# Kernel tuning notes

Hardware: AMD Instinct MI355X
Metric: run time of the kernel (lower is better)

Reference implementation:

```python
import jax, jax.numpy as jnp
import numpy as np

BS, RAL, LAL = 128, 1024, 256
CS, VOC, HFS, EMB = 256, 34, 512, 256


def setup_inputs() -> dict:
    key0 = jax.random.key(0)
    ks = jax.random.split(key0, 16)
    s = 0.02
    # mask from random valid lengths (at least 1 valid frame per example)
    lengths = jax.random.randint(ks[15], (BS,), RAL // 2, RAL + 1)
    mask = (jnp.arange(RAL)[None, :] < lengths[:, None]).astype(jnp.float32)
    return {
        "key": jax.random.normal(ks[0], (BS, RAL, CS), jnp.float32),
        "val": jax.random.normal(ks[1], (BS, RAL, CS), jnp.float32),
        "mask": mask,
        "emb": jax.random.normal(ks[2], (VOC, EMB), jnp.float32) * s,
        "Wih_a": jax.random.normal(ks[3], (4 * HFS, EMB + CS), jnp.float32) * s,
        "Whh_a": jax.random.normal(ks[4], (4 * HFS, HFS), jnp.float32) * s,
        "bih_a": jnp.zeros((4 * HFS,), jnp.float32),
        "bhh_a": jnp.zeros((4 * HFS,), jnp.float32),
        "Wih_b": jax.random.normal(ks[5], (4 * HFS, HFS), jnp.float32) * s,
        "Whh_b": jax.random.normal(ks[6], (4 * HFS, HFS), jnp.float32) * s,
        "bih_b": jnp.zeros((4 * HFS,), jnp.float32),
        "bhh_b": jnp.zeros((4 * HFS,), jnp.float32),
        "Wq": jax.random.normal(ks[7], (CS, HFS), jnp.float32) * s,
        "bq": jnp.zeros((CS,), jnp.float32),
        "Wc": jax.random.normal(ks[8], (VOC, HFS + CS), jnp.float32) * s,
        "bc": jnp.zeros((VOC,), jnp.float32),
        "y": jax.random.randint(ks[9], (BS, LAL), 0, VOC, jnp.int32),
    }


def _lstm_cell(x, h, c, Wih, Whh, bih, bhh):
    z = x @ Wih.T + bih + h @ Whh.T + bhh  # (BS, 4H)
    i, f, g, o = jnp.split(z, 4, axis=-1)
    i, f, o = jax.nn.sigmoid(i), jax.nn.sigmoid(f), jax.nn.sigmoid(o)
    g = jnp.tanh(g)
    c2 = f * c + i * g
    return o * jnp.tanh(c2), c2


def _attend(key, val, query, mask):
    # energy: (BS, RAL) = bmm(key, query[...,None])
    energy = jnp.einsum("brc,bc->br", key, query)
    att = jax.nn.softmax(energy, axis=1) * mask
    att = att / jnp.sum(att, axis=1, keepdims=True)
    return jnp.einsum("br,brc->bc", att, val)  # context (BS, CS)


def reference(key, val, mask, emb, Wih_a, Whh_a, bih_a, bhh_a,
              Wih_b, Whh_b, bih_b, bhh_b, Wq, bq, Wc, bc, y):
    bs = y.shape[0]
    z = jnp.zeros((bs, HFS), jnp.float32)
    init = (z, z, z, z, jnp.zeros((bs, CS), jnp.float32))

    def step(carry, y_t):
        ha, ca, hb, cb, ctx = carry
        e = emb[y_t]  # (BS, EMB)
        x = jnp.concatenate([e, ctx], axis=1)
        ha, ca = _lstm_cell(x, ha, ca, Wih_a, Whh_a, bih_a, bhh_a)
        hb, cb = _lstm_cell(ha, hb, cb, Wih_b, Whh_b, bih_b, bhh_b)
        query = hb @ Wq.T + bq  # (BS, CS)
        ctx = _attend(key, val, query, mask)
        logits = jnp.concatenate([hb, ctx], axis=1) @ Wc.T + bc  # (BS, VOC)
        return (ha, ca, hb, cb, ctx), logits

    _, preds = jax.lax.scan(step, init, y.T)  # (LAL, BS, VOC)
    return jnp.transpose(preds, (1, 0, 2))  # (BS, LAL, VOC)
```

## Files before the change

### kernel.cpp

```cpp
#include <hip/hip_runtime.h>
#include <cstdint>
#include <cstddef>

static constexpr int BS  = 128;
static constexpr int RAL = 1024;
static constexpr int LAL = 256;
static constexpr int CS  = 256;
static constexpr int VOC = 34;
static constexpr int HFS = 512;
static constexpr int EMB = 256;

static constexpr int NSPLIT = 2;
static constexpr int RSPL   = RAL / NSPLIT;
static constexpr int NBLK   = 256;

typedef float  f32x4  __attribute__((ext_vector_type(4)));
typedef short  bf16x8 __attribute__((ext_vector_type(8)));

#define SC_AGENT __HIP_MEMORY_SCOPE_AGENT

static __device__ __forceinline__ float bflo(unsigned int u) {
    return __builtin_bit_cast(float, u << 16);
}
static __device__ __forceinline__ float bfhi(unsigned int u) {
    return __builtin_bit_cast(float, u & 0xffff0000u);
}
static __device__ __forceinline__ unsigned short f2bf(float f) {
    unsigned int x = __builtin_bit_cast(unsigned int, f);
    x = (x + 0x7fffu + ((x >> 16) & 1u)) >> 16;
    return (unsigned short)x;
}
static __device__ __forceinline__ float bcf(unsigned u) { return __builtin_bit_cast(float, u); }
static __device__ __forceinline__ unsigned fcb(float f) { return __builtin_bit_cast(unsigned, f); }
static __device__ __forceinline__ float sigf(float x)   { return 1.0f / (1.0f + __expf(-x)); }
static __device__ __forceinline__ float tanhf_(float x) { return 1.0f - 2.0f / (__expf(2.0f * x) + 1.0f); }

static __device__ __forceinline__ unsigned ldu32(const void* p) {
    return __hip_atomic_load((const unsigned*)p, __ATOMIC_RELAXED, SC_AGENT);
}
static __device__ __forceinline__ unsigned long long ldu64(const void* p) {
    return __hip_atomic_load((const unsigned long long*)p, __ATOMIC_RELAXED, SC_AGENT);
}
static __device__ __forceinline__ void stu32(void* p, unsigned v) {
    __hip_atomic_store((unsigned*)p, v, __ATOMIC_RELAXED, SC_AGENT);
}
static __device__ __forceinline__ void stu64(void* p, unsigned long long v) {
    __hip_atomic_store((unsigned long long*)p, v, __ATOMIC_RELAXED, SC_AGENT);
}
static __device__ __forceinline__ bf16x8 ld_bf16x8_sys(const unsigned short* p) {
    union { unsigned long long q[2]; bf16x8 v; } u;
    u.q[0] = ldu64(p);
    u.q[1] = ldu64(p + 4);
    return u.v;
}
static __device__ __forceinline__ unsigned long long packbf4(float a, float b, float c, float d) {
    return (unsigned long long)f2bf(a)
         | ((unsigned long long)f2bf(b) << 16)
         | ((unsigned long long)f2bf(c) << 32)
         | ((unsigned long long)f2bf(d) << 48);
}

__global__ void cvt4_kernel(const float4* __restrict__ in, ushort4* __restrict__ out, int n4) {
    int i  = blockIdx.x * blockDim.x + threadIdx.x;
    int st = gridDim.x * blockDim.x;
    for (; i < n4; i += st) {
        float4 v = in[i];
        ushort4 o;
        o.x = f2bf(v.x); o.y = f2bf(v.y); o.z = f2bf(v.z); o.w = f2bf(v.w);
        out[i] = o;
    }
}

__global__ __launch_bounds__(256) void len_kernel(const float* __restrict__ mask,
                                                  int* __restrict__ Llen,
                                                  float* __restrict__ attS) {
    __shared__ int red[256];
    const int b = blockIdx.x, tid = threadIdx.x;
    int c = 0;
    for (int r = tid; r < RAL; r += 256) c += (mask[b * RAL + r] != 0.0f) ? 1 : 0;
    red[tid] = c;
    __syncthreads();
    for (int s = 128; s > 0; s >>= 1) {
        if (tid < s) red[tid] += red[tid + s];
        __syncthreads();
    }
    if (tid == 0) Llen[b] = red[0];
    if (tid < NSPLIT) attS[b * NSPLIT + tid] = 0.5f;
}

struct SmLstm {
    float zp[7][4][64][4];
    float hT[16][17];
};
struct SmAttn {
    float hb_l[HFS];
    float q_lds[CS];
    float e_lds[RSPL];
    float ctxp[8][CS];
    float red[16];
};
static constexpr size_t SMSZ = sizeof(SmLstm) > sizeof(SmAttn) ? sizeof(SmLstm) : sizeof(SmAttn);

struct PParams {
    const void* keyp; const void* valp;
    const int* Llen; const int* y;
    const unsigned short* embb;
    const unsigned short* WihA; const unsigned short* WhhA;
    const float* bihA; const float* bhhA;
    const unsigned short* WihB; const unsigned short* WhhB;
    const float* bihB; const float* bhhB;
    const unsigned short* Wqb; const float* bq;
    const float* Wc; const float* bc;
    unsigned short* ha; unsigned short* hbuf;
    float* ca; float* cbuf;
    float* attM; float* attS; float* attC;
    unsigned* grp; unsigned* root;
    float* outp;
};

static __device__ __forceinline__ void gbar(unsigned* grp, unsigned* root, int blk, int round) {
    asm volatile("s_waitcnt vmcnt(0) lgkmcnt(0)" ::: "memory");
    __syncthreads();
    if (threadIdx.x == 0) {
        unsigned* g = grp + (blk >> 4) * 32;
        unsigned old = __hip_atomic_fetch_add(g, 1u, __ATOMIC_RELAXED, SC_AGENT);
        if (old == (unsigned)(round * 16 + 15))
            __hip_atomic_fetch_add(root, 1u, __ATOMIC_RELAXED, SC_AGENT);
        const unsigned tgt = (unsigned)((round + 1) * 16);
        while (__hip_atomic_load(root, __ATOMIC_RELAXED, SC_AGENT) < tgt)
            __builtin_amdgcn_s_sleep(8);
    }
    __syncthreads();
}

static __device__ __forceinline__ bf16x8 ctx_merge8(const float* c0, const float* c1,
                                                    float w0, float w1) {
    union { unsigned short s[8]; bf16x8 v; } r;
#pragma unroll
    for (int g = 0; g < 4; ++g) {
        unsigned long long qa = ldu64(c0 + g * 2);
        unsigned long long qb = ldu64(c1 + g * 2);
        float ax = bcf((unsigned)qa), ay = bcf((unsigned)(qa >> 32));
        float bx = bcf((unsigned)qb), by = bcf((unsigned)(qb >> 32));
        r.s[g * 2 + 0] = f2bf(w0 * ax + w1 * bx);
        r.s[g * 2 + 1] = f2bf(w0 * ay + w1 * by);
    }
    return r.v;
}

template <bool ISA>
static __device__ __forceinline__ void lstm_phase(
    int blk, int tid,
    const unsigned short* xrow,
    const float* attM, const float* attS, const float* attC,
    const unsigned short* embb, const int* yidx, int t,
    const unsigned short* hIn,
    const unsigned short* Wih, const unsigned short* Whh,
    const float* bih, const float* bhh,
    float* cst, unsigned short* hout,
    SmLstm* sm)
{
    const int lane = tid & 63;
    const int wv   = tid >> 6;
    const int seg  = wv >> 1;
    const int sub  = wv & 1;
    const int quad = lane >> 4;
    const int l16  = lane & 15;
    const int jsl  = blk & 31;
    const int bgr  = blk >> 5;
    const int j    = jsl * 16 + l16;
    const int mrow = bgr * 16 + l16;
    const int off0 = sub * 128 + quad * 8;

    const unsigned short* arow = nullptr;
    const float* c0 = nullptr;
    float w0m = 0.0f, w1m = 0.0f;
    bool scA;
    if (seg >= 2) {
        arow = hIn + (long)mrow * HFS + (seg & 1) * 256 + off0;
        scA = true;
    } else if (!ISA) {
        arow = xrow + (long)mrow * HFS + (seg & 1) * 256 + off0;
        scA = true;
    } else if (seg == 0) {
        arow = embb + (long)yidx[mrow * LAL + t] * EMB + off0;
        scA = false;
    } else {
        c0 = attC + (long)mrow * NSPLIT * CS + off0;
        float M0 = bcf(ldu32(attM + mrow * 2)),     M1 = bcf(ldu32(attM + mrow * 2 + 1));
        float S0 = bcf(ldu32(attS + mrow * 2)),     S1 = bcf(ldu32(attS + mrow * 2 + 1));
        float mm = fmaxf(M0, M1);
        float e0 = __expf(M0 - mm), e1 = __expf(M1 - mm);
        float inv = 1.0f / (e0 * S0 + e1 * S1);
        w0m = e0 * inv; w1m = e1 * inv;
        scA = false;
    }

    const unsigned short* wb = ((seg < 2) ? Wih : Whh) + (seg & 1) * 256 + off0;
    const unsigned short* wg[4];
#pragma unroll
    for (int g = 0; g < 4; ++g) wg[g] = wb + (long)(g * HFS + j) * HFS;

    f32x4 acc[4];
#pragma unroll
    for (int g = 0; g < 4; ++g) acc[g] = (f32x4)0.0f;

#pragma unroll
    for (int kc = 0; kc < 4; ++kc) {
        bf16x8 a;
        if (scA)                 a = ld_bf16x8_sys(arow + kc * 32);
        else if (!ISA || seg == 0) a = *(const bf16x8*)(arow + kc * 32);
        else                     a = ctx_merge8(c0 + kc * 32, c0 + CS + kc * 32, w0m, w1m);
        bf16x8 b0 = *(const bf16x8*)(wg[0] + kc * 32);
        bf16x8 b1 = *(const bf16x8*)(wg[1] + kc * 32);
        bf16x8 b2 = *(const bf16x8*)(wg[2] + kc * 32);
        bf16x8 b3 = *(const bf16x8*)(wg[3] + kc * 32);
        acc[0] = __builtin_amdgcn_mfma_f32_16x16x32_bf16(a, b0, acc[0], 0, 0, 0);
        acc[1] = __builtin_amdgcn_mfma_f32_16x16x32_bf16(a, b1, acc[1], 0, 0, 0);
        acc[2] = __builtin_amdgcn_mfma_f32_16x16x32_bf16(a, b2, acc[2], 0, 0, 0);
        acc[3] = __builtin_amdgcn_mfma_f32_16x16x32_bf16(a, b3, acc[3], 0, 0, 0);
    }

    if (wv != 0) {
#pragma unroll
        for (int g = 0; g < 4; ++g)
            *(f32x4*)&sm->zp[wv - 1][g][lane][0] = acc[g];
    }
    __syncthreads();
    if (wv == 0) {
#pragma unroll
        for (int g = 0; g < 4; ++g) {
#pragma unroll
            for (int w = 0; w < 7; ++w)
                acc[g] += *(const f32x4*)&sm->zp[w][g][lane][0];
        }
        const float bI = bih[j]           + bhh[j];
        const float bF = bih[HFS + j]     + bhh[HFS + j];
        const float bG = bih[2 * HFS + j] + bhh[2 * HFS + j];
        const float bO = bih[3 * HFS + j] + bhh[3 * HFS + j];
#pragma unroll
        for (int r = 0; r < 4; ++r) {
            int m   = bgr * 16 + quad * 4 + r;
            int idx = m * HFS + j;
            float iv = sigf(acc[0][r] + bI);
            float fv = sigf(acc[1][r] + bF);
            float gv = tanhf_(acc[2][r] + bG);
            float ov = sigf(acc[3][r] + bO);
            float cn = fv * cst[idx] + iv * gv;
            cst[idx] = cn;
            sm->hT[quad * 4 + r][l16] = ov * tanhf_(cn);
        }
        float h0 = sm->hT[l16][quad * 4 + 0];
        float h1 = sm->hT[l16][quad * 4 + 1];
        float h2 = sm->hT[l16][quad * 4 + 2];
        float h3 = sm->hT[l16][quad * 4 + 3];
        stu64(hout + (long)(bgr * 16 + l16) * HFS + jsl * 16 + quad * 4,
              packbf4(h0, h1, h2, h3));
    }
}

template <bool KVBF>
static __device__ __forceinline__ void attn_phase(
    int blk, int tid,
    const void* keyp, const void* valp,
    const int* __restrict__ Llen,
    const unsigned short* __restrict__ hbv,
    const unsigned short* __restrict__ Wqb, const float* __restrict__ bq,
    float* __restrict__ attM, float* __restrict__ attS, float* __restrict__ attC,
    SmAttn* sm)
{
    const int b     = blk >> 1;
    const int sp    = blk & 1;
    const int L     = Llen[b];
    const int rhalf = (L + 1) >> 1;
    const int rbase = sp * rhalf;
    int nv = L - rbase;
    if (nv > rhalf) nv = rhalf;

    if (nv <= 0) {
        if (tid < CS) stu32(attC + ((long)b * NSPLIT + sp) * CS + tid, fcb(0.0f));
        if (tid == 0) {
            stu32(attM + b * NSPLIT + sp, fcb(-1e30f));
            stu32(attS + b * NSPLIT + sp, fcb(0.0f));
        }
        return;
    }

    if (tid < 128) {
        unsigned long long q = ldu64(hbv + (long)b * HFS + tid * 4);
        sm->hb_l[tid * 4 + 0] = bflo((unsigned)(q       ) & 0xffffu ? (unsigned)(q) & 0xffffu : 0u);
        sm->hb_l[tid * 4 + 0] = bflo((unsigned)(q        & 0xffffu));
        sm->hb_l[tid * 4 + 1] = bflo((unsigned)((q >> 16) & 0xffffu));
        sm->hb_l[tid * 4 + 2] = bflo((unsigned)((q >> 32) & 0xffffu));
        sm->hb_l[tid * 4 + 3] = bflo((unsigned)((q >> 48) & 0xffffu));
    }
    __syncthreads();

    {
        const int c  = tid >> 1;
        const int jj = tid & 1;
        const unsigned short* wr = Wqb + (long)c * HFS + jj * 256;
        const float* xr = &sm->hb_l[jj * 256];
        float qa = 0.0f;
#pragma unroll 8
        for (int k = 0; k < 256; k += 8) {
            uint4 u = *(const uint4*)(wr + k);
            float4 h0 = *(const float4*)(xr + k);
            float4 h1 = *(const float4*)(xr + k + 4);
            qa += bflo(u.x) * h0.x + bfhi(u.x) * h0.y
                + bflo(u.y) * h0.z + bfhi(u.y) * h0.w
                + bflo(u.z) * h1.x + bfhi(u.z) * h1.y
                + bflo(u.w) * h1.z + bfhi(u.w) * h1.w;
        }
        qa += __shfl_xor(qa, 1);
        if (jj == 0) sm->q_lds[c] = qa + bq[c];
    }
    __syncthreads();

    {
        const int jj   = tid & 7;
        const int rloc = tid >> 3;
        for (int r0 = 0; r0 < nv; r0 += 64) {
            const int r = r0 + rloc;
            float acc = 0.0f;
            if (r < nv) {
                if (KVBF) {
                    const unsigned short* kp = (const unsigned short*)keyp
                        + ((long)b * RAL + rbase + r) * CS + jj * 32;
#pragma unroll
                    for (int i = 0; i < 4; ++i) {
                        uint4 u = *(const uint4*)(kp + i * 8);
                        const float* qp = &sm->q_lds[jj * 32 + i * 8];
                        float4 qa  = *(const float4*)qp;
                        float4 qb2 = *(const float4*)(qp + 4);
                        acc += bflo(u.x) * qa.x  + bfhi(u.x) * qa.y
                             + bflo(u.y) * qa.z  + bfhi(u.y) * qa.w
                             + bflo(u.z) * qb2.x + bfhi(u.z) * qb2.y
                             + bflo(u.w) * qb2.z + bfhi(u.w) * qb2.w;
                    }
                } else {
                    const float* kp = (const float*)keyp
                        + ((long)b * RAL + rbase + r) * CS + jj * 32;
#pragma unroll
                    for (int i = 0; i < 8; ++i) {
                        float4 kv = *(const float4*)(kp + i * 4);
                        float4 qa = *(const float4*)&sm->q_lds[jj * 32 + i * 4];
                        acc += kv.x * qa.x + kv.y * qa.y + kv.z * qa.z + kv.w * qa.w;
                    }
                }
            }
            acc += __shfl_xor(acc, 1);
            acc += __shfl_xor(acc, 2);
            acc += __shfl_xor(acc, 4);
            if (jj == 0 && r < nv) sm->e_lds[r] = acc;
        }
    }
    __syncthreads();

    float pm = (tid < nv) ? sm->e_lds[tid] : -1e30f;
#pragma unroll
    for (int s = 32; s > 0; s >>= 1) pm = fmaxf(pm, __shfl_xor(pm, s));
    if ((tid & 63) == 0) sm->red[tid >> 6] = pm;
    __syncthreads();
    float M = sm->red[0];
#pragma unroll
    for (int i = 1; i < 8; ++i) M = fmaxf(M, sm->red[i]);

    float ps = 0.0f;
    if (tid < nv) { float v = __expf(sm->e_lds[tid] - M); sm->e_lds[tid] = v; ps = v; }
#pragma unroll
    for (int s = 32; s > 0; s >>= 1) ps += __shfl_xor(ps, s);
    if ((tid & 63) == 0) sm->red[8 + (tid >> 6)] = ps;
    __syncthreads();
    float S = 0.0f;
#pragma unroll
    for (int i = 0; i < 8; ++i) S += sm->red[8 + i];

    if (tid == 0) {
        stu32(attM + b * NSPLIT + sp, fcb(M));
        stu32(attS + b * NSPLIT + sp, fcb(S));
    }

    {
        const int wv = tid >> 6;
        const int c4 = (tid & 63) * 4;
        float a0 = 0.f, a1 = 0.f, a2 = 0.f, a3 = 0.f;
        if (KVBF) {
            const unsigned short* vb = (const unsigned short*)valp
                + ((long)b * RAL + rbase) * CS + c4;
            int r = wv;
            for (; r + 24 < nv; r += 32) {
                uint2 u0 = *(const uint2*)(vb + (long)(r)      * CS);
                uint2 u1 = *(const uint2*)(vb + (long)(r + 8)  * CS);
                uint2 u2 = *(const uint2*)(vb + (long)(r + 16) * CS);
                uint2 u3 = *(const uint2*)(vb + (long)(r + 24) * CS);
                float w0 = sm->e_lds[r],      w1 = sm->e_lds[r + 8];
                float w2 = sm->e_lds[r + 16], w3 = sm->e_lds[r + 24];
                a0 += w0 * bflo(u0.x) + w1 * bflo(u1.x) + w2 * bflo(u2.x) + w3 * bflo(u3.x);
                a1 += w0 * bfhi(u0.x) + w1 * bfhi(u1.x) + w2 * bfhi(u2.x) + w3 * bfhi(u3.x);
                a2 += w0 * bflo(u0.y) + w1 * bflo(u1.y) + w2 * bflo(u2.y) + w3 * bflo(u3.y);
                a3 += w0 * bfhi(u0.y) + w1 * bfhi(u1.y) + w2 * bfhi(u2.y) + w3 * bfhi(u3.y);
            }
            for (; r < nv; r += 8) {
                uint2 u = *(const uint2*)(vb + (long)r * CS);
                float w = sm->e_lds[r];
                a0 += w * bflo(u.x); a1 += w * bfhi(u.x);
                a2 += w * bflo(u.y); a3 += w * bfhi(u.y);
            }
        } else {
            const float* vb = (const float*)valp + ((long)b * RAL + rbase) * CS + c4;
            int r = wv;
            for (; r + 24 < nv; r += 32) {
                float4 v0 = *(const float4*)(vb + (long)(r)      * CS);
                float4 v1 = *(const float4*)(vb + (long)(r + 8)  * CS);
                float4 v2 = *(const float4*)(vb + (long)(r + 16) * CS);
                float4 v3 = *(const float4*)(vb + (long)(r + 24) * CS);
                float w0 = sm->e_lds[r],      w1 = sm->e_lds[r + 8];
                float w2 = sm->e_lds[r + 16], w3 = sm->e_lds[r + 24];
                a0 += w0 * v0.x + w1 * v1.x + w2 * v2.x + w3 * v3.x;
                a1 += w0 * v0.y + w1 * v1.y + w2 * v2.y + w3 * v3.y;
                a2 += w0 * v0.z + w1 * v1.z + w2 * v2.z + w3 * v3.z;
                a3 += w0 * v0.w + w1 * v1.w + w2 * v2.w + w3 * v3.w;
            }
            for (; r < nv; r += 8) {
                float4 v = *(const float4*)(vb + (long)r * CS);
                float w = sm->e_lds[r];
                a0 += w * v.x; a1 += w * v.y; a2 += w * v.z; a3 += w * v.w;
            }
        }
        float4 out4 = {a0, a1, a2, a3};
        *(float4*)&sm->ctxp[tid >> 6][c4] = out4;
    }
    __syncthreads();

    if (tid < CS) {
        float cv = 0.0f;
#pragma unroll
        for (int w = 0; w < 8; ++w) cv += sm->ctxp[w][tid];
        stu32(attC + ((long)b * NSPLIT + sp) * CS + tid, fcb(cv));
    }
}

static __device__ __forceinline__ void logits_phase(
    int blk, int tid,
    const unsigned short* __restrict__ hb,
    const float* __restrict__ attM, const float* __restrict__ attS,
    const float* __restrict__ attC,
    const float* __restrict__ Wc, const float* __restrict__ bc,
    float* __restrict__ outp, int tOut)
{
    const int bgr  = blk >> 5;
    const int vsl  = blk & 31;
    const int bloc = tid >> 5;
    const int jj   = tid & 31;
    const int b    = bgr * 16 + bloc;

    float M0 = bcf(ldu32(attM + b * 2)),     M1 = bcf(ldu32(attM + b * 2 + 1));
    float S0 = bcf(ldu32(attS + b * 2)),     S1 = bcf(ldu32(attS + b * 2 + 1));
    float mm = fmaxf(M0, M1);
    float w0 = __expf(M0 - mm), w1 = __expf(M1 - mm);
    float inv = 1.0f / (w0 * S0 + w1 * S1);
    w0 *= inv; w1 *= inv;

    float xh[16];
    const unsigned short* hp = hb + (long)b * HFS + jj * 16;
#pragma unroll
    for (int g = 0; g < 4; ++g) {
        unsigned long long q = ldu64(hp + g * 4);
        xh[g * 4 + 0] = bflo((unsigned)( q        & 0xffffu));
        xh[g * 4 + 1] = bflo((unsigned)((q >> 16) & 0xffffu));
        xh[g * 4 + 2] = bflo((unsigned)((q >> 32) & 0xffffu));
        xh[g * 4 + 3] = bflo((unsigned)((q >> 48) & 0xffffu));
    }
    float xc[8];
    const float* c0 = attC + ((long)b * NSPLIT + 0) * CS + jj * 8;
    const float* c1 = attC + ((long)b * NSPLIT + 1) * CS + jj * 8;
#pragma unroll
    for (int g = 0; g < 4; ++g) {
        unsigned long long qa = ldu64(c0 + g * 2);
        unsigned long long qb = ldu64(c1 + g * 2);
        xc[g * 2 + 0] = w0 * bcf((unsigned)qa)         + w1 * bcf((unsigned)qb);
        xc[g * 2 + 1] = w0 * bcf((unsigned)(qa >> 32)) + w1 * bcf((unsigned)(qb >> 32));
    }

#pragma unroll
    for (int vv = 0; vv < 2; ++vv) {
        int v = vsl + vv * 32;
        if (v >= VOC) break;
        const float* wr = Wc + (long)v * (HFS + CS);
        float part = 0.0f;
#pragma unroll
        for (int g = 0; g < 4; ++g) {
            float4 wv4 = *(const float4*)(wr + jj * 16 + g * 4);
            part += wv4.x * xh[g * 4 + 0] + wv4.y * xh[g * 4 + 1]
                  + wv4.z * xh[g * 4 + 2] + wv4.w * xh[g * 4 + 3];
        }
#pragma unroll
        for (int g = 0; g < 2; ++g) {
            float4 wv4 = *(const float4*)(wr + HFS + jj * 8 + g * 4);
            part += wv4.x * xc[g * 4 + 0] + wv4.y * xc[g * 4 + 1]
                  + wv4.z * xc[g * 4 + 2] + wv4.w * xc[g * 4 + 3];
        }
        part += __shfl_xor(part, 1);
        part += __shfl_xor(part, 2);
        part += __shfl_xor(part, 4);
        part += __shfl_xor(part, 8);
        part += __shfl_xor(part, 16);
        if (jj == 0)
            outp[((long)b * LAL + tOut) * VOC + v] = part + bc[v];
    }
}

template <bool KVBF>
__global__ __launch_bounds__(512) void fused_kernel(PParams P)
{
    __shared__ __align__(16) unsigned char smraw[SMSZ];
    SmLstm* smL = (SmLstm*)smraw;
    SmAttn* smA = (SmAttn*)smraw;

    const int blk = blockIdx.x;
    const int tid = threadIdx.x;
    int round = 0;

    for (int t = 0; t < LAL; ++t) {
        const unsigned short* haIn  = P.ha   + (t & 1) * (BS * HFS);
        unsigned short*       haOut = P.ha   + ((t + 1) & 1) * (BS * HFS);
        const unsigned short* hbIn  = P.hbuf + (t & 1) * (BS * HFS);
        unsigned short*       hbOut = P.hbuf + ((t + 1) & 1) * (BS * HFS);

        lstm_phase<true>(blk, tid, nullptr, P.attM, P.attS, P.attC,
                         P.embb, P.y, t, haIn,
                         P.WihA, P.WhhA, P.bihA, P.bhhA, P.ca, haOut, smL);
        gbar(P.grp, P.root, blk, round++);

        if (t > 0)
            logits_phase(blk, tid, hbIn, P.attM, P.attS, P.attC, P.Wc, P.bc, P.outp, t - 1);
        lstm_phase<false>(blk, tid, haOut, nullptr, nullptr, nullptr,
                          nullptr, nullptr, t, hbIn,
                          P.WihB, P.WhhB, P.bihB, P.bhhB, P.cbuf, hbOut, smL);
        gbar(P.grp, P.root, blk, round++);

        attn_phase<KVBF>(blk, tid, P.keyp, P.valp, P.Llen, hbOut,
                         P.Wqb, P.bq, P.attM, P.attS, P.attC, smA);
        gbar(P.grp, P.root, blk, round++);
    }
    logits_phase(blk, tid, P.hbuf + (LAL & 1) * (BS * HFS),
                 P.attM, P.attS, P.attC, P.Wc, P.bc, P.outp, LAL - 1);
}

extern "C" void kernel_launch(void* const* d_in, const int* in_sizes, int n_in,
                              void* d_out, int out_size, void* d_ws, size_t ws_size,
                              hipStream_t stream)
{
    (void)in_sizes; (void)n_in; (void)out_size;
    const float* keyf  = (const float*)d_in[0];
    const float* valf  = (const float*)d_in[1];
    const float* mask  = (const float*)d_in[2];
    const float* embf  = (const float*)d_in[3];
    const float* WihAf = (const float*)d_in[4];
    const float* WhhAf = (const float*)d_in[5];
    const float* bihA  = (const float*)d_in[6];
    const float* bhhA  = (const float*)d_in[7];
    const float* WihBf = (const float*)d_in[8];
    const float* WhhBf = (const float*)d_in[9];
    const float* bihB  = (const float*)d_in[10];
    const float* bhhB  = (const float*)d_in[11];
    const float* Wqf   = (const float*)d_in[12];
    const float* bq    = (const float*)d_in[13];
    const float* Wc    = (const float*)d_in[14];
    const float* bc    = (const float*)d_in[15];
    const int*   y     = (const int*)d_in[16];
    float* outp = (float*)d_out;

    size_t off = 0;
    auto take = [&](size_t bytes) -> void* {
        void* p = (char*)d_ws + off;
        off += (bytes + 255) & ~(size_t)255;
        return p;
    };

    unsigned short* ha    = (unsigned short*)take((size_t)2 * BS * HFS * 2);
    unsigned short* hbuf  = (unsigned short*)take((size_t)2 * BS * HFS * 2);
    float*          ca    = (float*)take((size_t)BS * HFS * 4);
    float*          cbuf  = (float*)take((size_t)BS * HFS * 4);
    float*          attM  = (float*)take((size_t)BS * NSPLIT * 4);
    float*          attS  = (float*)take((size_t)BS * NSPLIT * 4);
    float*          attC  = (float*)take((size_t)BS * NSPLIT * CS * 4);
    unsigned*       grp   = (unsigned*)take((size_t)16 * 32 * 4);
    unsigned*       root  = (unsigned*)take((size_t)32 * 4);
    size_t stateBytes = off;

    int*            Llen  = (int*)take((size_t)BS * 4);
    unsigned short* embb  = (unsigned short*)take((size_t)VOC * EMB * 2);
    unsigned short* WihAb = (unsigned short*)take((size_t)4 * HFS * HFS * 2);
    unsigned short* WhhAb = (unsigned short*)take((size_t)4 * HFS * HFS * 2);
    unsigned short* WihBb = (unsigned short*)take((size_t)4 * HFS * HFS * 2);
    unsigned short* WhhBb = (unsigned short*)take((size_t)4 * HFS * HFS * 2);
    unsigned short* Wqb   = (unsigned short*)take((size_t)CS * HFS * 2);

    const size_t kvBytes = (size_t)BS * RAL * CS * 2;
    unsigned short* keyb = nullptr;
    unsigned short* valb = nullptr;
    bool kvbf = false;
    bool keyInVal = false;
    if (off + 2 * (kvBytes + 256) <= ws_size) {
        keyb = (unsigned short*)take(kvBytes);
        valb = (unsigned short*)take(kvBytes);
        kvbf = true;
    } else if (off + kvBytes + 256 <= ws_size) {
        valb = (unsigned short*)take(kvBytes);
        keyb = (unsigned short*)d_in[1];
        kvbf = true;
        keyInVal = true;
    }

    hipMemsetAsync(d_ws, 0, stateBytes, stream);
    len_kernel<<<dim3(BS), dim3(256), 0, stream>>>(mask, Llen, attS);

    auto cvt = [&](const float* src, unsigned short* dst, long n) {
        int n4 = (int)(n / 4);
        int blocks = (n4 + 255) / 256;
        if (blocks > 8192) blocks = 8192;
        cvt4_kernel<<<dim3(blocks), dim3(256), 0, stream>>>((const float4*)src, (ushort4*)dst, n4);
    };
    cvt(embf,  embb,  (long)VOC * EMB);
    cvt(WihAf, WihAb, (long)4 * HFS * HFS);
    cvt(WhhAf, WhhAb, (long)4 * HFS * HFS);
    cvt(WihBf, WihBb, (long)4 * HFS * HFS);
    cvt(WhhBf, WhhBb, (long)4 * HFS * HFS);
    cvt(Wqf,   Wqb,   (long)CS * HFS);
    if (kvbf) {
        if (keyInVal) {
            cvt(valf, valb, (long)BS * RAL * CS);
            cvt(keyf, keyb, (long)BS * RAL * CS);
        } else {
            cvt(keyf, keyb, (long)BS * RAL * CS);
            cvt(valf, valb, (long)BS * RAL * CS);
        }
    }

    PParams prm;
    prm.keyp = kvbf ? (const void*)keyb : (const void*)keyf;
    prm.valp = kvbf ? (const void*)valb : (const void*)valf;
    prm.Llen = Llen; prm.y = y;
    prm.embb = embb;
    prm.WihA = WihAb; prm.WhhA = WhhAb; prm.bihA = bihA; prm.bhhA = bhhA;
    prm.WihB = WihBb; prm.WhhB = WhhBb; prm.bihB = bihB; prm.bhhB = bhhB;
    prm.Wqb = Wqb; prm.bq = bq; prm.Wc = Wc; prm.bc = bc;
    prm.ha = ha; prm.hbuf = hbuf; prm.ca = ca; prm.cbuf = cbuf;
    prm.attM = attM; prm.attS = attS; prm.attC = attC;
    prm.grp = grp; prm.root = root;
    prm.outp = outp;

    void* kargs[] = { &prm };
    if (kvbf)
        hipLaunchCooperativeKernel(reinterpret_cast<void*>(&fused_kernel<true>),
                                   dim3(NBLK), dim3(512), kargs, 0, stream);
    else
        hipLaunchCooperativeKernel(reinterpret_cast<void*>(&fused_kernel<false>),
                                   dim3(NBLK), dim3(512), kargs, 0, stream);
}
```

Before: 13.00 ms.

## Double block size, add KV cache-warming waves and split query GEMM into MFMA phase

```diff
diff --git a/kernel.cpp b/kernel.cpp
--- a/kernel.cpp
+++ b/kernel.cpp
@@ -85,7 +85,7 @@
         __syncthreads();
     }
     if (tid == 0) Llen[b] = red[0];
-    if (tid < NSPLIT) attS[b * NSPLIT + tid] = 0.5f;
+    if (tid < NSPLIT) attS[b * NSPLIT + tid] = 1.0f / NSPLIT;
 }
 
 struct SmLstm {
@@ -93,11 +93,10 @@
     float hT[16][17];
 };
 struct SmAttn {
-    float hb_l[HFS];
     float q_lds[CS];
     float e_lds[RSPL];
-    float ctxp[8][CS];
-    float red[16];
+    float ctxp[32][CS];
+    float red[32];
 };
 static constexpr size_t SMSZ = sizeof(SmLstm) > sizeof(SmAttn) ? sizeof(SmLstm) : sizeof(SmAttn);
 
@@ -114,6 +113,7 @@
     unsigned short* ha; unsigned short* hbuf;
     float* ca; float* cbuf;
     float* attM; float* attS; float* attC;
+    float* qbuf;
     unsigned* grp; unsigned* root;
     float* outp;
 };
@@ -133,19 +133,43 @@
     __syncthreads();
 }
 
-static __device__ __forceinline__ bf16x8 ctx_merge8(const float* c0, const float* c1,
-                                                    float w0, float w1) {
+static __device__ __forceinline__ bf16x8 ctx_merge8(const float* cb, const float* wm) {
     union { unsigned short s[8]; bf16x8 v; } r;
 #pragma unroll
-    for (int g = 0; g < 4; ++g) {
-        unsigned long long qa = ldu64(c0 + g * 2);
-        unsigned long long qb = ldu64(c1 + g * 2);
-        float ax = bcf((unsigned)qa), ay = bcf((unsigned)(qa >> 32));
-        float bx = bcf((unsigned)qb), by = bcf((unsigned)(qb >> 32));
-        r.s[g * 2 + 0] = f2bf(w0 * ax + w1 * bx);
-        r.s[g * 2 + 1] = f2bf(w0 * ay + w1 * by);
+    for (int e = 0; e < 8; e += 2) {
+        float x0 = 0.f, x1 = 0.f;
+#pragma unroll
+        for (int s2 = 0; s2 < NSPLIT; ++s2) {
+            unsigned long long q = ldu64(cb + (long)s2 * CS + e);
+            x0 += wm[s2] * bcf((unsigned)q);
+            x1 += wm[s2] * bcf((unsigned)(q >> 32));
+        }
+        r.s[e]     = f2bf(x0);
+        r.s[e + 1] = f2bf(x1);
     }
     return r.v;
+}
+
+template <bool KVBF>
+static __device__ __forceinline__ void kv_touch(int blk, const void* ptr,
+                                                const int* __restrict__ Llen,
+                                                int rr, int rstride, int cc, int budget)
+{
+    if (!KVBF) return;
+    const int b = blk >> 1, sp = blk & 1;
+    const int L = Llen[b];
+    const int rhalf = (L + 1) >> 1;
+    const int rbase = sp * rhalf;
+    int nv = L - rbase; if (nv > rhalf) nv = rhalf;
+    if (nv > budget) nv = budget;
+    const uint4* kp = (const uint4*)((const unsigned short*)ptr
+                      + ((long)b * RAL + rbase) * CS) + cc;
+    unsigned acc = 0;
+    for (int r = rr; r < nv; r += rstride) {
+        uint4 u = kp[(long)r * 32];
+        acc ^= u.x ^ u.y ^ u.z ^ u.w;
+    }
+    asm volatile("" :: "v"(acc));
 }
 
 template <bool ISA>
@@ -162,69 +186,82 @@
 {
     const int lane = tid & 63;
     const int wv   = tid >> 6;
-    const int seg  = wv >> 1;
-    const int sub  = wv & 1;
+    const bool act = (wv < 8);
     const int quad = lane >> 4;
     const int l16  = lane & 15;
     const int jsl  = blk & 31;
     const int bgr  = blk >> 5;
     const int j    = jsl * 16 + l16;
     const int mrow = bgr * 16 + l16;
-    const int off0 = sub * 128 + quad * 8;
-
-    const unsigned short* arow = nullptr;
-    const float* c0 = nullptr;
-    float w0m = 0.0f, w1m = 0.0f;
-    bool scA;
-    if (seg >= 2) {
-        arow = hIn + (long)mrow * HFS + (seg & 1) * 256 + off0;
-        scA = true;
-    } else if (!ISA) {
-        arow = xrow + (long)mrow * HFS + (seg & 1) * 256 + off0;
-        scA = true;
-    } else if (seg == 0) {
-        arow = embb + (long)yidx[mrow * LAL + t] * EMB + off0;
-        scA = false;
-    } else {
-        c0 = attC + (long)mrow * NSPLIT * CS + off0;
-        float M0 = bcf(ldu32(attM + mrow * 2)),     M1 = bcf(ldu32(attM + mrow * 2 + 1));
-        float S0 = bcf(ldu32(attS + mrow * 2)),     S1 = bcf(ldu32(attS + mrow * 2 + 1));
-        float mm = fmaxf(M0, M1);
-        float e0 = __expf(M0 - mm), e1 = __expf(M1 - mm);
-        float inv = 1.0f / (e0 * S0 + e1 * S1);
-        w0m = e0 * inv; w1m = e1 * inv;
-        scA = false;
-    }
-
-    const unsigned short* wb = ((seg < 2) ? Wih : Whh) + (seg & 1) * 256 + off0;
-    const unsigned short* wg[4];
-#pragma unroll
-    for (int g = 0; g < 4; ++g) wg[g] = wb + (long)(g * HFS + j) * HFS;
 
     f32x4 acc[4];
 #pragma unroll
     for (int g = 0; g < 4; ++g) acc[g] = (f32x4)0.0f;
 
-#pragma unroll
-    for (int kc = 0; kc < 4; ++kc) {
-        bf16x8 a;
-        if (scA)                 a = ld_bf16x8_sys(arow + kc * 32);
-        else if (!ISA || seg == 0) a = *(const bf16x8*)(arow + kc * 32);
-        else                     a = ctx_merge8(c0 + kc * 32, c0 + CS + kc * 32, w0m, w1m);
-        bf16x8 b0 = *(const bf16x8*)(wg[0] + kc * 32);
-        bf16x8 b1 = *(const bf16x8*)(wg[1] + kc * 32);
-        bf16x8 b2 = *(const bf16x8*)(wg[2] + kc * 32);
-        bf16x8 b3 = *(const bf16x8*)(wg[3] + kc * 32);
-        acc[0] = __builtin_amdgcn_mfma_f32_16x16x32_bf16(a, b0, acc[0], 0, 0, 0);
-        acc[1] = __builtin_amdgcn_mfma_f32_16x16x32_bf16(a, b1, acc[1], 0, 0, 0);
-        acc[2] = __builtin_amdgcn_mfma_f32_16x16x32_bf16(a, b2, acc[2], 0, 0, 0);
-        acc[3] = __builtin_amdgcn_mfma_f32_16x16x32_bf16(a, b3, acc[3], 0, 0, 0);
-    }
-
-    if (wv != 0) {
-#pragma unroll
-        for (int g = 0; g < 4; ++g)
-            *(f32x4*)&sm->zp[wv - 1][g][lane][0] = acc[g];
+    if (act) {
+        const int seg  = wv >> 1;
+        const int sub  = wv & 1;
+        const int off0 = sub * 128 + quad * 8;
+
+        const unsigned short* arow = nullptr;
+        const float* c0 = nullptr;
+        float wm[NSPLIT];
+        bool scA;
+        if (seg >= 2) {
+            arow = hIn + (long)mrow * HFS + (seg & 1) * 256 + off0;
+            scA = true;
+        } else if (!ISA) {
+            arow = xrow + (long)mrow * HFS + (seg & 1) * 256 + off0;
+            scA = true;
+        } else if (seg == 0) {
+            arow = embb + (long)yidx[mrow * LAL + t] * EMB + off0;
+            scA = false;
+        } else {
+            c0 = attC + (long)mrow * NSPLIT * CS + off0;
+            float Ms[NSPLIT], Ss[NSPLIT];
+#pragma unroll
+            for (int s = 0; s < NSPLIT; ++s) {
+                Ms[s] = bcf(ldu32(attM + mrow * NSPLIT + s));
+                Ss[s] = bcf(ldu32(attS + mrow * NSPLIT + s));
+            }
+            float mm = Ms[0];
+#pragma unroll
+            for (int s = 1; s < NSPLIT; ++s) mm = fmaxf(mm, Ms[s]);
+            float den = 0.f;
+#pragma unroll
+            for (int s = 0; s < NSPLIT; ++s) { wm[s] = __expf(Ms[s] - mm); den += wm[s] * Ss[s]; }
+            float inv = 1.0f / den;
+#pragma unroll
+            for (int s = 0; s < NSPLIT; ++s) wm[s] *= inv;
+            scA = false;
+        }
+
+        const unsigned short* wb = ((seg < 2) ? Wih : Whh) + (seg & 1) * 256 + off0;
+        const unsigned short* wg[4];
+#pragma unroll
+        for (int g = 0; g < 4; ++g) wg[g] = wb + (long)(g * HFS + j) * HFS;
+
+#pragma unroll
+        for (int kc = 0; kc < 4; ++kc) {
+            bf16x8 a;
+            if (scA)                   a = ld_bf16x8_sys(arow + kc * 32);
+            else if (!ISA || seg == 0) a = *(const bf16x8*)(arow + kc * 32);
+            else                       a = ctx_merge8(c0 + kc * 32, wm);
+            bf16x8 b0 = *(const bf16x8*)(wg[0] + kc * 32);
+            bf16x8 b1 = *(const bf16x8*)(wg[1] + kc * 32);
+            bf16x8 b2 = *(const bf16x8*)(wg[2] + kc * 32);
+            bf16x8 b3 = *(const bf16x8*)(wg[3] + kc * 32);
+            acc[0] = __builtin_amdgcn_mfma_f32_16x16x32_bf16(a, b0, acc[0], 0, 0, 0);
+            acc[1] = __builtin_amdgcn_mfma_f32_16x16x32_bf16(a, b1, acc[1], 0, 0, 0);
+            acc[2] = __builtin_amdgcn_mfma_f32_16x16x32_bf16(a, b2, acc[2], 0, 0, 0);
+            acc[3] = __builtin_amdgcn_mfma_f32_16x16x32_bf16(a, b3, acc[3], 0, 0, 0);
+        }
+
+        if (wv != 0) {
+#pragma unroll
+            for (int g = 0; g < 4; ++g)
+                *(f32x4*)&sm->zp[wv - 1][g][lane][0] = acc[g];
+        }
     }
     __syncthreads();
     if (wv == 0) {
@@ -259,13 +296,55 @@
     }
 }
 
+static __device__ __forceinline__ void qcalc_phase(
+    int blk, int tid,
+    const unsigned short* hb,
+    const unsigned short* Wqb, const float* bq,
+    float* qbuf, SmLstm* sm)
+{
+    const int lane = tid & 63;
+    const int wv   = tid >> 6;
+    const bool act = (wv < 8);
+    const int quad = lane >> 4;
+    const int l16  = lane & 15;
+    const int mt   = blk >> 4;
+    const int nt   = blk & 15;
+
+    f32x4 acc = (f32x4)0.0f;
+    if (act) {
+        const int mrow = mt * 16 + l16;
+        const int c    = nt * 16 + l16;
+        const int koff = wv * 64 + quad * 8;
+        const unsigned short* ar = hb  + (long)mrow * HFS + koff;
+        const unsigned short* br = Wqb + (long)c    * HFS + koff;
+#pragma unroll
+        for (int kc = 0; kc < 2; ++kc) {
+            bf16x8 a = ld_bf16x8_sys(ar + kc * 32);
+            bf16x8 b = *(const bf16x8*)(br + kc * 32);
+            acc = __builtin_amdgcn_mfma_f32_16x16x32_bf16(a, b, acc, 0, 0, 0);
+        }
+        if (wv != 0) *(f32x4*)&sm->zp[wv - 1][0][lane][0] = acc;
+    }
+    __syncthreads();
+    if (wv == 0) {
+#pragma unroll
+        for (int w = 0; w < 7; ++w) acc += *(const f32x4*)&sm->zp[w][0][lane][0];
+        const int c = nt * 16 + l16;
+        const float bqv = bq[c];
+#pragma unroll
+        for (int r = 0; r < 4; ++r) {
+            int b2 = mt * 16 + quad * 4 + r;
+            stu32(qbuf + (long)b2 * CS + c, fcb(acc[r] + bqv));
+        }
+    }
+}
+
 template <bool KVBF>
 static __device__ __forceinline__ void attn_phase(
     int blk, int tid,
     const void* keyp, const void* valp,
     const int* __restrict__ Llen,
-    const unsigned short* __restrict__ hbv,
-    const unsigned short* __restrict__ Wqb, const float* __restrict__ bq,
+    const float* __restrict__ qbuf,
     float* __restrict__ attM, float* __restrict__ attS, float* __restrict__ attC,
     SmAttn* sm)
 {
@@ -286,51 +365,23 @@
         return;
     }
 
-    if (tid < 128) {
-        unsigned long long q = ldu64(hbv + (long)b * HFS + tid * 4);
-        sm->hb_l[tid * 4 + 0] = bflo((unsigned)(q       ) & 0xffffu ? (unsigned)(q) & 0xffffu : 0u);
-        sm->hb_l[tid * 4 + 0] = bflo((unsigned)(q        & 0xffffu));
-        sm->hb_l[tid * 4 + 1] = bflo((unsigned)((q >> 16) & 0xffffu));
-        sm->hb_l[tid * 4 + 2] = bflo((unsigned)((q >> 32) & 0xffffu));
-        sm->hb_l[tid * 4 + 3] = bflo((unsigned)((q >> 48) & 0xffffu));
-    }
+    if (tid < CS) sm->q_lds[tid] = bcf(ldu32(qbuf + (long)b * CS + tid));
     __syncthreads();
 
     {
-        const int c  = tid >> 1;
-        const int jj = tid & 1;
-        const unsigned short* wr = Wqb + (long)c * HFS + jj * 256;
-        const float* xr = &sm->hb_l[jj * 256];
-        float qa = 0.0f;
-#pragma unroll 8
-        for (int k = 0; k < 256; k += 8) {
-            uint4 u = *(const uint4*)(wr + k);
-            float4 h0 = *(const float4*)(xr + k);
-            float4 h1 = *(const float4*)(xr + k + 4);
-            qa += bflo(u.x) * h0.x + bfhi(u.x) * h0.y
-                + bflo(u.y) * h0.z + bfhi(u.y) * h0.w
-                + bflo(u.z) * h1.x + bfhi(u.z) * h1.y
-                + bflo(u.w) * h1.z + bfhi(u.w) * h1.w;
-        }
-        qa += __shfl_xor(qa, 1);
-        if (jj == 0) sm->q_lds[c] = qa + bq[c];
-    }
-    __syncthreads();
-
-    {
-        const int jj   = tid & 7;
-        const int rloc = tid >> 3;
-        for (int r0 = 0; r0 < nv; r0 += 64) {
+        const int jj   = tid & 3;
+        const int rloc = tid >> 2;
+        for (int r0 = 0; r0 < nv; r0 += 256) {
             const int r = r0 + rloc;
             float acc = 0.0f;
             if (r < nv) {
                 if (KVBF) {
                     const unsigned short* kp = (const unsigned short*)keyp
-                        + ((long)b * RAL + rbase + r) * CS + jj * 32;
-#pragma unroll
-                    for (int i = 0; i < 4; ++i) {
+                        + ((long)b * RAL + rbase + r) * CS + jj * 64;
+#pragma unroll
+                    for (int i = 0; i < 8; ++i) {
                         uint4 u = *(const uint4*)(kp + i * 8);
-                        const float* qp = &sm->q_lds[jj * 32 + i * 8];
+                        const float* qp = &sm->q_lds[jj * 64 + i * 8];
                         float4 qa  = *(const float4*)qp;
                         float4 qb2 = *(const float4*)(qp + 4);
                         acc += bflo(u.x) * qa.x  + bfhi(u.x) * qa.y
@@ -340,18 +391,17 @@
                     }
                 } else {
                     const float* kp = (const float*)keyp
-                        + ((long)b * RAL + rbase + r) * CS + jj * 32;
-#pragma unroll
-                    for (int i = 0; i < 8; ++i) {
+                        + ((long)b * RAL + rbase + r) * CS + jj * 64;
+#pragma unroll
+                    for (int i = 0; i < 16; ++i) {
                         float4 kv = *(const float4*)(kp + i * 4);
-                        float4 qa = *(const float4*)&sm->q_lds[jj * 32 + i * 4];
+                        float4 qa = *(const float4*)&sm->q_lds[jj * 64 + i * 4];
                         acc += kv.x * qa.x + kv.y * qa.y + kv.z * qa.z + kv.w * qa.w;
                     }
                 }
             }
             acc += __shfl_xor(acc, 1);
             acc += __shfl_xor(acc, 2);
-            acc += __shfl_xor(acc, 4);
             if (jj == 0 && r < nv) sm->e_lds[r] = acc;
         }
     }
@@ -364,17 +414,17 @@
     __syncthreads();
     float M = sm->red[0];
 #pragma unroll
-    for (int i = 1; i < 8; ++i) M = fmaxf(M, sm->red[i]);
+    for (int i = 1; i < 16; ++i) M = fmaxf(M, sm->red[i]);
 
     float ps = 0.0f;
     if (tid < nv) { float v = __expf(sm->e_lds[tid] - M); sm->e_lds[tid] = v; ps = v; }
 #pragma unroll
     for (int s = 32; s > 0; s >>= 1) ps += __shfl_xor(ps, s);
-    if ((tid & 63) == 0) sm->red[8 + (tid >> 6)] = ps;
+    if ((tid & 63) == 0) sm->red[16 + (tid >> 6)] = ps;
     __syncthreads();
     float S = 0.0f;
 #pragma unroll
-    for (int i = 0; i < 8; ++i) S += sm->red[8 + i];
+    for (int i = 0; i < 16; ++i) S += sm->red[16 + i];
 
     if (tid == 0) {
         stu32(attM + b * NSPLIT + sp, fcb(M));
@@ -382,61 +432,88 @@
     }
 
     {
-        const int wv = tid >> 6;
-        const int c4 = (tid & 63) * 4;
-        float a0 = 0.f, a1 = 0.f, a2 = 0.f, a3 = 0.f;
+        const int rg = tid >> 5;
+        const int c8 = (tid & 31) * 8;
+        float a0=0.f,a1=0.f,a2=0.f,a3=0.f,a4=0.f,a5=0.f,a6=0.f,a7=0.f;
         if (KVBF) {
             const unsigned short* vb = (const unsigned short*)valp
-                + ((long)b * RAL + rbase) * CS + c4;
-            int r = wv;
-            for (; r + 24 < nv; r += 32) {
-                uint2 u0 = *(const uint2*)(vb + (long)(r)      * CS);
-                uint2 u1 = *(const uint2*)(vb + (long)(r + 8)  * CS);
-                uint2 u2 = *(const uint2*)(vb + (long)(r + 16) * CS);
-                uint2 u3 = *(const uint2*)(vb + (long)(r + 24) * CS);
-                float w0 = sm->e_lds[r],      w1 = sm->e_lds[r + 8];
-                float w2 = sm->e_lds[r + 16], w3 = sm->e_lds[r + 24];
-                a0 += w0 * bflo(u0.x) + w1 * bflo(u1.x) + w2 * bflo(u2.x) + w3 * bflo(u3.x);
-                a1 += w0 * bfhi(u0.x) + w1 * bfhi(u1.x) + w2 * bfhi(u2.x) + w3 * bfhi(u3.x);
-                a2 += w0 * bflo(u0.y) + w1 * bflo(u1.y) + w2 * bflo(u2.y) + w3 * bflo(u3.y);
-                a3 += w0 * bfhi(u0.y) + w1 * bfhi(u1.y) + w2 * bfhi(u2.y) + w3 * bfhi(u3.y);
+                + ((long)b * RAL + rbase) * CS + c8;
+            int r = rg;
+            for (; r + 224 < nv; r += 256) {
+                uint4 u[8]; float w[8];
+#pragma unroll
+                for (int k = 0; k < 8; ++k) u[k] = *(const uint4*)(vb + (long)(r + 32 * k) * CS);
+#pragma unroll
+                for (int k = 0; k < 8; ++k) w[k] = sm->e_lds[r + 32 * k];
+#pragma unroll
+                for (int k = 0; k < 8; ++k) {
+                    a0 += w[k] * bflo(u[k].x); a1 += w[k] * bfhi(u[k].x);
+                    a2 += w[k] * bflo(u[k].y); a3 += w[k] * bfhi(u[k].y);
+                    a4 += w[k] * bflo(u[k].z); a5 += w[k] * bfhi(u[k].z);
+                    a6 += w[k] * bflo(u[k].w); a7 += w[k] * bfhi(u[k].w);
+                }
             }
-            for (; r < nv; r += 8) {
-                uint2 u = *(const uint2*)(vb + (long)r * CS);
+            for (; r + 96 < nv; r += 128) {
+                uint4 u[4]; float w[4];
+#pragma unroll
+                for (int k = 0; k < 4; ++k) u[k] = *(const uint4*)(vb + (long)(r + 32 * k) * CS);
+#pragma unroll
+                for (int k = 0; k < 4; ++k) w[k] = sm->e_lds[r + 32 * k];
+#pragma unroll
+                for (int k = 0; k < 4; ++k) {
+                    a0 += w[k] * bflo(u[k].x); a1 += w[k] * bfhi(u[k].x);
+                    a2 += w[k] * bflo(u[k].y); a3 += w[k] * bfhi(u[k].y);
+                    a4 += w[k] * bflo(u[k].z); a5 += w[k] * bfhi(u[k].z);
+                    a6 += w[k] * bflo(u[k].w); a7 += w[k] * bfhi(u[k].w);
+                }
+            }
+            for (; r < nv; r += 32) {
+                uint4 u = *(const uint4*)(vb + (long)r * CS);
                 float w = sm->e_lds[r];
                 a0 += w * bflo(u.x); a1 += w * bfhi(u.x);
                 a2 += w * bflo(u.y); a3 += w * bfhi(u.y);
+                a4 += w * bflo(u.z); a5 += w * bfhi(u.z);
+                a6 += w * bflo(u.w); a7 += w * bfhi(u.w);
             }
         } else {
-            const float* vb = (const float*)valp + ((long)b * RAL + rbase) * CS + c4;
-            int r = wv;
-            for (; r + 24 < nv; r += 32) {
-                float4 v0 = *(const float4*)(vb + (long)(r)      * CS);
-                float4 v1 = *(const float4*)(vb + (long)(r + 8)  * CS);
-                float4 v2 = *(const float4*)(vb + (long)(r + 16) * CS);
-                float4 v3 = *(const float4*)(vb + (long)(r + 24) * CS);
-                float w0 = sm->e_lds[r],      w1 = sm->e_lds[r + 8];
-                float w2 = sm->e_lds[r + 16], w3 = sm->e_lds[r + 24];
-                a0 += w0 * v0.x + w1 * v1.x + w2 * v2.x + w3 * v3.x;
-                a1 += w0 * v0.y + w1 * v1.y + w2 * v2.y + w3 * v3.y;
-                a2 += w0 * v0.z + w1 * v1.z + w2 * v2.z + w3 * v3.z;
-                a3 += w0 * v0.w + w1 * v1.w + w2 * v2.w + w3 * v3.w;
+            const float* vb = (const float*)valp + ((long)b * RAL + rbase) * CS + c8;
+            int r = rg;
+            for (; r + 96 < nv; r += 128) {
+                float4 v0[4], v1[4]; float w[4];
+#pragma unroll
+                for (int k = 0; k < 4; ++k) {
+                    v0[k] = *(const float4*)(vb + (long)(r + 32 * k) * CS);
+                    v1[k] = *(const float4*)(vb + (long)(r + 32 * k) * CS + 4);
+                }
+#pragma unroll
+                for (int k = 0; k < 4; ++k) w[k] = sm->e_lds[r + 32 * k];
+#pragma unroll
+                for (int k = 0; k < 4; ++k) {
+                    a0 += w[k] * v0[k].x; a1 += w[k] * v0[k].y;
+                    a2 += w[k] * v0[k].z; a3 += w[k] * v0[k].w;
+                    a4 += w[k] * v1[k].x; a5 += w[k] * v1[k].y;
+                    a6 += w[k] * v1[k].z; a7 += w[k] * v1[k].w;
+                }
             }
-            for (; r < nv; r += 8) {
-                float4 v = *(const float4*)(vb + (long)r * CS);
+            for (; r < nv; r += 32) {
+                float4 v0 = *(const float4*)(vb + (long)r * CS);
+                float4 v1 = *(const float4*)(vb + (long)r * CS + 4);
                 float w = sm->e_lds[r];
-                a0 += w * v.x; a1 += w * v.y; a2 += w * v.z; a3 += w * v.w;
+                a0 += w * v0.x; a1 += w * v0.y; a2 += w * v0.z; a3 += w * v0.w;
+                a4 += w * v1.x; a5 += w * v1.y; a6 += w * v1.z; a7 += w * v1.w;
             }
         }
-        float4 out4 = {a0, a1, a2, a3};
-        *(float4*)&sm->ctxp[tid >> 6][c4] = out4;
+        float4 o0 = {a0, a1, a2, a3};
+        float4 o1 = {a4, a5, a6, a7};
+        *(float4*)&sm->ctxp[rg][c8]     = o0;
+        *(float4*)&sm->ctxp[rg][c8 + 4] = o1;
     }
     __syncthreads();
 
     if (tid < CS) {
         float cv = 0.0f;
 #pragma unroll
-        for (int w = 0; w < 8; ++w) cv += sm->ctxp[w][tid];
+        for (int g = 0; g < 32; ++g) cv += sm->ctxp[g][tid];
         stu32(attC + ((long)b * NSPLIT + sp) * CS + tid, fcb(cv));
     }
 }
@@ -455,12 +532,21 @@
     const int jj   = tid & 31;
     const int b    = bgr * 16 + bloc;
 
-    float M0 = bcf(ldu32(attM + b * 2)),     M1 = bcf(ldu32(attM + b * 2 + 1));
-    float S0 = bcf(ldu32(attS + b * 2)),     S1 = bcf(ldu32(attS + b * 2 + 1));
-    float mm = fmaxf(M0, M1);
-    float w0 = __expf(M0 - mm), w1 = __expf(M1 - mm);
-    float inv = 1.0f / (w0 * S0 + w1 * S1);
-    w0 *= inv; w1 *= inv;
+    float Ms[NSPLIT], Ss[NSPLIT], wgt[NSPLIT];
+#pragma unroll
+    for (int s = 0; s < NSPLIT; ++s) {
+        Ms[s] = bcf(ldu32(attM + b * NSPLIT + s));
+        Ss[s] = bcf(ldu32(attS + b * NSPLIT + s));
+    }
+    float mm = Ms[0];
+#pragma unroll
+    for (int s = 1; s < NSPLIT; ++s) mm = fmaxf(mm, Ms[s]);
+    float den = 0.f;
+#pragma unroll
+    for (int s = 0; s < NSPLIT; ++s) { wgt[s] = __expf(Ms[s] - mm); den += wgt[s] * Ss[s]; }
+    float inv = 1.0f / den;
+#pragma unroll
+    for (int s = 0; s < NSPLIT; ++s) wgt[s] *= inv;
 
     float xh[16];
     const unsigned short* hp = hb + (long)b * HFS + jj * 16;
@@ -473,14 +559,18 @@
         xh[g * 4 + 3] = bflo((unsigned)((q >> 48) & 0xffffu));
     }
     float xc[8];
-    const float* c0 = attC + ((long)b * NSPLIT + 0) * CS + jj * 8;
-    const float* c1 = attC + ((long)b * NSPLIT + 1) * CS + jj * 8;
+    const float* cb = attC + (long)b * NSPLIT * CS + jj * 8;
 #pragma unroll
     for (int g = 0; g < 4; ++g) {
-        unsigned long long qa = ldu64(c0 + g * 2);
-        unsigned long long qb = ldu64(c1 + g * 2);
-        xc[g * 2 + 0] = w0 * bcf((unsigned)qa)         + w1 * bcf((unsigned)qb);
-        xc[g * 2 + 1] = w0 * bcf((unsigned)(qa >> 32)) + w1 * bcf((unsigned)(qb >> 32));
+        float x0 = 0.f, x1 = 0.f;
+#pragma unroll
+        for (int s = 0; s < NSPLIT; ++s) {
+            unsigned long long q = ldu64(cb + (long)s * CS + g * 2);
+            x0 += wgt[s] * bcf((unsigned)q);
+            x1 += wgt[s] * bcf((unsigned)(q >> 32));
+        }
+        xc[g * 2]     = x0;
+        xc[g * 2 + 1] = x1;
     }
 
 #pragma unroll
@@ -512,7 +602,7 @@
 }
 
 template <bool KVBF>
-__global__ __launch_bounds__(512) void fused_kernel(PParams P)
+__global__ __launch_bounds__(1024, 4) void fused_kernel(PParams P)
 {
     __shared__ __align__(16) unsigned char smraw[SMSZ];
     SmLstm* smL = (SmLstm*)smraw;
@@ -520,6 +610,7 @@
 
     const int blk = blockIdx.x;
     const int tid = threadIdx.x;
+    const int wv  = tid >> 6;
     int round = 0;
 
     for (int t = 0; t < LAL; ++t) {
@@ -528,24 +619,37 @@
         const unsigned short* hbIn  = P.hbuf + (t & 1) * (BS * HFS);
         unsigned short*       hbOut = P.hbuf + ((t + 1) & 1) * (BS * HFS);
 
+        if (wv >= 8)
+            kv_touch<KVBF>(blk, P.keyp, P.Llen, (tid - 512) >> 5, 16, (tid - 512) & 31, 160);
         lstm_phase<true>(blk, tid, nullptr, P.attM, P.attS, P.attC,
                          P.embb, P.y, t, haIn,
                          P.WihA, P.WhhA, P.bihA, P.bhhA, P.ca, haOut, smL);
         gbar(P.grp, P.root, blk, round++);
 
-        if (t > 0)
-            logits_phase(blk, tid, hbIn, P.attM, P.attS, P.attC, P.Wc, P.bc, P.outp, t - 1);
+        if (wv >= 8 && t > 0)
+            logits_phase(blk, tid - 512, hbIn, P.attM, P.attS, P.attC,
+                         P.Wc, P.bc, P.outp, t - 1);
         lstm_phase<false>(blk, tid, haOut, nullptr, nullptr, nullptr,
                           nullptr, nullptr, t, hbIn,
                           P.WihB, P.WhhB, P.bihB, P.bhhB, P.cbuf, hbOut, smL);
         gbar(P.grp, P.root, blk, round++);
 
-        attn_phase<KVBF>(blk, tid, P.keyp, P.valp, P.Llen, hbOut,
-                         P.Wqb, P.bq, P.attM, P.attS, P.attC, smA);
+        if (blk < 128) {
+            if (wv >= 8)
+                kv_touch<KVBF>(blk, P.valp, P.Llen, (tid - 512) >> 5, 16, (tid - 512) & 31, 64);
+            qcalc_phase(blk, tid, hbOut, P.Wqb, P.bq, P.qbuf, smL);
+        } else {
+            kv_touch<KVBF>(blk, P.valp, P.Llen, tid >> 5, 32, tid & 31, 128);
+        }
         gbar(P.grp, P.root, blk, round++);
-    }
-    logits_phase(blk, tid, P.hbuf + (LAL & 1) * (BS * HFS),
-                 P.attM, P.attS, P.attC, P.Wc, P.bc, P.outp, LAL - 1);
+
+        attn_phase<KVBF>(blk, tid, P.keyp, P.valp, P.Llen,
+                         P.qbuf, P.attM, P.attS, P.attC, smA);
+        gbar(P.grp, P.root, blk, round++);
+    }
+    if (tid < 512)
+        logits_phase(blk, tid, P.hbuf + (LAL & 1) * (BS * HFS),
+                     P.attM, P.attS, P.attC, P.Wc, P.bc, P.outp, LAL - 1);
 }
 
 extern "C" void kernel_launch(void* const* d_in, const int* in_sizes, int n_in,
@@ -586,6 +690,7 @@
     float*          attM  = (float*)take((size_t)BS * NSPLIT * 4);
     float*          attS  = (float*)take((size_t)BS * NSPLIT * 4);
     float*          attC  = (float*)take((size_t)BS * NSPLIT * CS * 4);
+    float*          qbuf  = (float*)take((size_t)BS * CS * 4);
     unsigned*       grp   = (unsigned*)take((size_t)16 * 32 * 4);
     unsigned*       root  = (unsigned*)take((size_t)32 * 4);
     size_t stateBytes = off;
@@ -649,14 +754,15 @@
     prm.Wqb = Wqb; prm.bq = bq; prm.Wc = Wc; prm.bc = bc;
     prm.ha = ha; prm.hbuf = hbuf; prm.ca = ca; prm.cbuf = cbuf;
     prm.attM = attM; prm.attS = attS; prm.attC = attC;
+    prm.qbuf = qbuf;
     prm.grp = grp; prm.root = root;
     prm.outp = outp;
 
     void* kargs[] = { &prm };
     if (kvbf)
         hipLaunchCooperativeKernel(reinterpret_cast<void*>(&fused_kernel<true>),
-                                   dim3(NBLK), dim3(512), kargs, 0, stream);
+                                   dim3(NBLK), dim3(1024), kargs, 0, stream);
     else
         hipLaunchCooperativeKernel(reinterpret_cast<void*>(&fused_kernel<false>),
-                                   dim3(NBLK), dim3(512), kargs, 0, stream);
-}
+                                   dim3(NBLK), dim3(1024), kargs, 0, stream);
+}
```

Result: slower. 17.66 ms (+35.8%).
